# Optimization experiments

Measured on AMD Instinct MI355X. Metric: run time of the kernel, lower is better.

Reference implementation:

```python
import jax, jax.numpy as jnp
import numpy as np

N_NODES = 50000
N_EDGES = 800000
D_IN = 128
D_HID = 16
N_CLS = 3


def setup_inputs() -> dict:
    key = jax.random.key(0)
    k = jax.random.split(key, 8)
    x = jax.random.normal(k[0], (N_NODES, D_IN), dtype=jnp.float32)
    edge_index = jax.random.randint(k[1], (2, N_EDGES), 0, N_NODES, dtype=jnp.int64)
    # SAGEConv params: lin_l (applied to aggregated neighbors, has bias),
    # lin_r (applied to root node, no bias) -- PyG defaults with mean aggregation.
    s1 = 1.0 / np.sqrt(D_IN)
    s2 = 1.0 / np.sqrt(D_HID)
    W1_l = jax.random.normal(k[2], (D_HID, D_IN), dtype=jnp.float32) * s1
    b1_l = jnp.zeros((D_HID,), dtype=jnp.float32)
    W1_r = jax.random.normal(k[3], (D_HID, D_IN), dtype=jnp.float32) * s1
    W2_l = jax.random.normal(k[4], (N_CLS, D_HID), dtype=jnp.float32) * s2
    b2_l = jnp.zeros((N_CLS,), dtype=jnp.float32)
    W2_r = jax.random.normal(k[5], (N_CLS, D_HID), dtype=jnp.float32) * s2
    return {"x": x, "edge_index": edge_index, "W1_l": W1_l, "b1_l": b1_l,
            "W1_r": W1_r, "W2_l": W2_l, "b2_l": b2_l, "W2_r": W2_r}


def _mean_aggregate(x, src, dst, num_nodes):
    # messages x_j = x[src] scattered to dst, mean-reduced (PyG SAGEConv aggr='mean')
    summed = jax.ops.segment_sum(x[src], dst, num_segments=num_nodes)  # [N, D]
    counts = jax.ops.segment_sum(jnp.ones((src.shape[0],), dtype=x.dtype), dst,
                                 num_segments=num_nodes)
    return summed / jnp.maximum(counts, 1.0)[:, None]


def _sage_conv(x, src, dst, W_l, b_l, W_r, num_nodes):
    agg = _mean_aggregate(x, src, dst, num_nodes)
    return agg @ W_l.T + b_l + x @ W_r.T


def reference(x, edge_index, W1_l, b1_l, W1_r, W2_l, b2_l, W2_r):
    src, dst = edge_index[0], edge_index[1]
    n = x.shape[0]
    h = jax.nn.relu(_sage_conv(x, src, dst, W1_l, b1_l, W1_r, n))
    h = jax.nn.relu(_sage_conv(h, src, dst, W2_l, b2_l, W2_r, n))
    return jax.nn.log_softmax(h, axis=1)
```

## Files before the change

kernel.cpp:

```cpp
#include <hip/hip_runtime.h>
#include <math.h>

#define D_IN 128
#define N_CLS 3
#define NXCD 8
#define CAPU 64

__global__ __launch_bounds__(256) void zero_kernel(int* __restrict__ p, int n)
{
    int i = blockIdx.x * 256 + threadIdx.x;
    if (i < n) p[i] = 0;
}

__global__ __launch_bounds__(256) void pack_kernel(
    const int* __restrict__ src, const int* __restrict__ dstv,
    unsigned int* __restrict__ packed, int n_edges)
{
    int e = blockIdx.x * 256 + threadIdx.x;
    if (e < n_edges)
        packed[e] = ((unsigned)dstv[e] << 16) | (unsigned)src[e];
}

__global__ __launch_bounds__(256) void fused3_kernel(
    const float* __restrict__ x, const float* __restrict__ W1l,
    const float* __restrict__ W1r, float* __restrict__ y_l,
    float* __restrict__ y_r,
    const unsigned int* __restrict__ packed,
    int* __restrict__ deg, unsigned short* __restrict__ padadj,
    int n_edges, int n8, int n_nodes, int nblk)
{
    __shared__ float ws[32 * 132];
    const int t = threadIdx.x;

    for (int m = t; m < (32 * 128) / 4; m += 256) {
        int f = m * 4;
        int row = f >> 7, col = f & 127;
        const float* srcw = (row < 16) ? (W1l + row * 128 + col)
                                       : (W1r + (row - 16) * 128 + col);
        *(float4*)&ws[row * 132 + col] = *(const float4*)srcw;
    }
    __syncthreads();

    if (t < 128) {
        const int xg = blockIdx.x & (NXCD - 1);
        const int q  = blockIdx.x >> 3;
        const unsigned lo = (unsigned)(xg * n8);
        unsigned hi = lo + (unsigned)n8;
        if (hi > (unsigned)n_nodes) hi = (unsigned)n_nodes;
        const int gpb = nblk >> 3;
        const int stride = gpb * 128;
        const int e4n = n_edges >> 2;
        for (int i = q * 128 + t; i < e4n; i += stride) {
            uint4 p4 = *(const uint4*)&packed[i * 4];
            unsigned d, s;
            d = p4.x >> 16; s = p4.x & 0xFFFFu;
            if (d >= lo && d < hi) {
                int r = atomicAdd(&deg[d], 1);
                if (r < CAPU) padadj[(size_t)d * CAPU + r] = (unsigned short)s;
            }
            d = p4.y >> 16; s = p4.y & 0xFFFFu;
            if (d >= lo && d < hi) {
                int r = atomicAdd(&deg[d], 1);
                if (r < CAPU) padadj[(size_t)d * CAPU + r] = (unsigned short)s;
            }
            d = p4.z >> 16; s = p4.z & 0xFFFFu;
            if (d >= lo && d < hi) {
                int r = atomicAdd(&deg[d], 1);
                if (r < CAPU) padadj[(size_t)d * CAPU + r] = (unsigned short)s;
            }
            d = p4.w >> 16; s = p4.w & 0xFFFFu;
            if (d >= lo && d < hi) {
                int r = atomicAdd(&deg[d], 1);
                if (r < CAPU) padadj[(size_t)d * CAPU + r] = (unsigned short)s;
            }
        }
        if (q == 0 && t < (n_edges & 3)) {
            int e = (e4n << 2) + t;
            unsigned p = packed[e];
            unsigned d = p >> 16, s = p & 0xFFFFu;
            if (d >= lo && d < hi) {
                int r = atomicAdd(&deg[d], 1);
                if (r < CAPU) padadj[(size_t)d * CAPU + r] = (unsigned short)s;
            }
        }
        return;
    }

    const int tt = t - 128;
    const int ng = tt >> 3;
    const int og = tt & 7;
    const int node = blockIdx.x * 16 + ng;
    if (node >= n_nodes) return;

    const float4* xp = (const float4*)(x + (size_t)node * D_IN);
    float acc[4] = {0.f, 0.f, 0.f, 0.f};
    for (int k4 = 0; k4 < 32; ++k4) {
        float4 xv = xp[k4];
        const int kb = k4 * 4;
        #pragma unroll
        for (int j = 0; j < 4; ++j) {
            float4 wv = *(const float4*)&ws[(og + 8 * j) * 132 + kb];
            acc[j] = fmaf(xv.x, wv.x, acc[j]);
            acc[j] = fmaf(xv.y, wv.y, acc[j]);
            acc[j] = fmaf(xv.z, wv.z, acc[j]);
            acc[j] = fmaf(xv.w, wv.w, acc[j]);
        }
    }
    #pragma unroll
    for (int j = 0; j < 4; ++j) {
        int col = og + 8 * j;
        if (col < 16) y_l[(size_t)node * 16 + col] = acc[j];
        else          y_r[(size_t)node * 16 + (col - 16)] = acc[j];
    }
}

__global__ __launch_bounds__(256) void gather1u_kernel(
    const int* __restrict__ deg, const unsigned short* __restrict__ padadj,
    const float* __restrict__ y_l, const float* __restrict__ y_r,
    const float* __restrict__ b1, const float* __restrict__ W2l,
    const float* __restrict__ W2r, float* __restrict__ z_l,
    float* __restrict__ z_r, int n_nodes, int n8)
{
    const int t = threadIdx.x;
    const int c = t & 15;
    const int xg = blockIdx.x & (NXCD - 1);
    const int q = blockIdx.x >> 3;
    const int local = q * 16 + (t >> 4);
    if (local >= n8) return;
    const int n = xg * n8 + local;
    if (n >= n_nodes) return;

    const int dc = deg[n];
    const int dcl = dc < CAPU ? dc : CAPU;
    const unsigned short* ap = padadj + (size_t)n * CAPU;
    float acc = 0.f;
    int j = 0;
    for (; j + 8 <= dcl; j += 8) {
        uint4 v = *(const uint4*)(ap + j);
        int i0 = v.x & 0xFFFF, i1 = v.x >> 16;
        int i2 = v.y & 0xFFFF, i3 = v.y >> 16;
        int i4 = v.z & 0xFFFF, i5 = v.z >> 16;
        int i6 = v.w & 0xFFFF, i7 = v.w >> 16;
        float a0 = y_l[(size_t)i0 * 16 + c];
        float a1 = y_l[(size_t)i1 * 16 + c];
        float a2 = y_l[(size_t)i2 * 16 + c];
        float a3 = y_l[(size_t)i3 * 16 + c];
        float a4 = y_l[(size_t)i4 * 16 + c];
        float a5 = y_l[(size_t)i5 * 16 + c];
        float a6 = y_l[(size_t)i6 * 16 + c];
        float a7 = y_l[(size_t)i7 * 16 + c];
        acc += ((a0 + a1) + (a2 + a3)) + ((a4 + a5) + (a6 + a7));
    }
    for (; j < dcl; ++j) acc += y_l[(size_t)ap[j] * 16 + c];

    float inv = 1.0f / fmaxf((float)dc, 1.0f);
    float h = fmaxf(fmaf(acc, inv, b1[c] + y_r[(size_t)n * 16 + c]), 0.f);

    float zl[N_CLS], zr[N_CLS];
    #pragma unroll
    for (int o = 0; o < N_CLS; ++o) {
        float pl = h * W2l[o * 16 + c];
        float pr = h * W2r[o * 16 + c];
        #pragma unroll
        for (int d = 1; d < 16; d <<= 1) {
            pl += __shfl_xor(pl, d, 64);
            pr += __shfl_xor(pr, d, 64);
        }
        zl[o] = pl; zr[o] = pr;
    }
    if (c == 0) {
        *(float4*)&z_l[(size_t)n * 4] = make_float4(zl[0], zl[1], zl[2], 0.f);
        *(float4*)&z_r[(size_t)n * 4] = make_float4(zr[0], zr[1], zr[2], 0.f);
    }
}

__global__ __launch_bounds__(256) void gather2u_out_kernel(
    const int* __restrict__ deg, const unsigned short* __restrict__ padadj,
    const float* __restrict__ z_l, const float* __restrict__ z_r,
    const float* __restrict__ b2, float* __restrict__ out,
    int n_nodes, int n8)
{
    const int xg = blockIdx.x & (NXCD - 1);
    const int q = blockIdx.x >> 3;
    const int local = q * 256 + threadIdx.x;
    if (local >= n8) return;
    const int n = xg * n8 + local;
    if (n >= n_nodes) return;

    const int dc = deg[n];
    const int dcl = dc < CAPU ? dc : CAPU;
    const unsigned short* ap = padadj + (size_t)n * CAPU;
    float a0 = 0.f, a1 = 0.f, a2 = 0.f;
    int j = 0;
    for (; j + 8 <= dcl; j += 8) {
        uint4 v = *(const uint4*)(ap + j);
        int i0 = v.x & 0xFFFF, i1 = v.x >> 16;
        int i2 = v.y & 0xFFFF, i3 = v.y >> 16;
        int i4 = v.z & 0xFFFF, i5 = v.z >> 16;
        int i6 = v.w & 0xFFFF, i7 = v.w >> 16;
        float4 v0 = *(const float4*)&z_l[(size_t)i0 * 4];
        float4 v1 = *(const float4*)&z_l[(size_t)i1 * 4];
        float4 v2 = *(const float4*)&z_l[(size_t)i2 * 4];
        float4 v3 = *(const float4*)&z_l[(size_t)i3 * 4];
        float4 v4 = *(const float4*)&z_l[(size_t)i4 * 4];
        float4 v5 = *(const float4*)&z_l[(size_t)i5 * 4];
        float4 v6 = *(const float4*)&z_l[(size_t)i6 * 4];
        float4 v7 = *(const float4*)&z_l[(size_t)i7 * 4];
        a0 += ((v0.x + v1.x) + (v2.x + v3.x)) + ((v4.x + v5.x) + (v6.x + v7.x));
        a1 += ((v0.y + v1.y) + (v2.y + v3.y)) + ((v4.y + v5.y) + (v6.y + v7.y));
        a2 += ((v0.z + v1.z) + (v2.z + v3.z)) + ((v4.z + v5.z) + (v6.z + v7.z));
    }
    for (; j < dcl; ++j) {
        float4 v = *(const float4*)&z_l[(size_t)ap[j] * 4];
        a0 += v.x; a1 += v.y; a2 += v.z;
    }
    float inv = 1.0f / fmaxf((float)dc, 1.0f);
    float4 r = *(const float4*)&z_r[(size_t)n * 4];
    float v0 = fmaxf(fmaf(a0, inv, b2[0] + r.x), 0.f);
    float v1 = fmaxf(fmaf(a1, inv, b2[1] + r.y), 0.f);
    float v2 = fmaxf(fmaf(a2, inv, b2[2] + r.z), 0.f);
    float m = fmaxf(fmaxf(v0, v1), v2);
    float s = expf(v0 - m) + expf(v1 - m) + expf(v2 - m);
    float lse = m + logf(s);
    out[(size_t)n * 3 + 0] = v0 - lse;
    out[(size_t)n * 3 + 1] = v1 - lse;
    out[(size_t)n * 3 + 2] = v2 - lse;
}


__global__ __launch_bounds__(128) void lin1_kernel(
    const float* __restrict__ x, const float* __restrict__ W1l,
    const float* __restrict__ W1r, float* __restrict__ y_l,
    float* __restrict__ y_r, int* __restrict__ deg, int n_nodes)
{
    __shared__ float xs[64 * 132];
    __shared__ float ws[32 * 132];
    const int t = threadIdx.x;
    const int node0 = blockIdx.x * 64;

    {
        int i = blockIdx.x * 128 + t;
        if (i < n_nodes) deg[i] = 0;
    }

    for (int m = t; m < (32 * 128) / 4; m += 128) {
        int f = m * 4;
        int row = f >> 7, col = f & 127;
        const float* srcw = (row < 16) ? (W1l + row * 128 + col)
                                       : (W1r + (row - 16) * 128 + col);
        *(float4*)&ws[row * 132 + col] = *(const float4*)srcw;
    }
    for (int m = t; m < (64 * 128) / 4; m += 128) {
        int f = m * 4;
        int row = f >> 7, col = f & 127;
        int node = node0 + row;
        float4 g = make_float4(0.f, 0.f, 0.f, 0.f);
        if (node < n_nodes) g = *(const float4*)(x + (size_t)node * D_IN + col);
        *(float4*)&xs[row * 132 + col] = g;
    }
    __syncthreads();

    const int ng = t >> 3;
    const int og = t & 7;
    float acc[4][4];
    #pragma unroll
    for (int i = 0; i < 4; ++i)
        #pragma unroll
        for (int j = 0; j < 4; ++j) acc[i][j] = 0.f;

    for (int k = 0; k < 128; k += 4) {
        float4 xv[4], wv[4];
        #pragma unroll
        for (int i = 0; i < 4; ++i)
            xv[i] = *(const float4*)&xs[(ng + 16 * i) * 132 + k];
        #pragma unroll
        for (int j = 0; j < 4; ++j)
            wv[j] = *(const float4*)&ws[(og + 8 * j) * 132 + k];
        #pragma unroll
        for (int i = 0; i < 4; ++i)
            #pragma unroll
            for (int j = 0; j < 4; ++j) {
                acc[i][j] = fmaf(xv[i].x, wv[j].x, acc[i][j]);
                acc[i][j] = fmaf(xv[i].y, wv[j].y, acc[i][j]);
                acc[i][j] = fmaf(xv[i].z, wv[j].z, acc[i][j]);
                acc[i][j] = fmaf(xv[i].w, wv[j].w, acc[i][j]);
            }
    }

    #pragma unroll
    for (int i = 0; i < 4; ++i) {
        int node = node0 + ng + 16 * i;
        if (node >= n_nodes) continue;
        #pragma unroll
        for (int j = 0; j < 4; ++j) {
            int col = og + 8 * j;
            if (col < 16) y_l[(size_t)node * 16 + col] = acc[i][j];
            else          y_r[(size_t)node * 16 + (col - 16)] = acc[i][j];
        }
    }
}

__global__ __launch_bounds__(256) void fillx_kernel(
    const int* __restrict__ src, const int* __restrict__ dst,
    int* __restrict__ deg, int* __restrict__ padadj,
    int n_edges, int cap, int n8, int n_nodes, int bpx)
{
    const int xg = blockIdx.x & (NXCD - 1);
    const int q  = blockIdx.x >> 3;
    const int lo = xg * n8;
    int hi = lo + n8; if (hi > n_nodes) hi = n_nodes;
    const int stride = bpx * 256;

    const int e4n = n_edges >> 2;
    for (int i = q * 256 + threadIdx.x; i < e4n; i += stride) {
        int4 d4 = *(const int4*)&dst[i * 4];
        if (d4.x >= lo && d4.x < hi) {
            int r = atomicAdd(&deg[d4.x], 1);
            if (r < cap) padadj[(size_t)d4.x * cap + r] = src[i * 4 + 0];
        }
        if (d4.y >= lo && d4.y < hi) {
            int r = atomicAdd(&deg[d4.y], 1);
            if (r < cap) padadj[(size_t)d4.y * cap + r] = src[i * 4 + 1];
        }
        if (d4.z >= lo && d4.z < hi) {
            int r = atomicAdd(&deg[d4.z], 1);
            if (r < cap) padadj[(size_t)d4.z * cap + r] = src[i * 4 + 2];
        }
        if (d4.w >= lo && d4.w < hi) {
            int r = atomicAdd(&deg[d4.w], 1);
            if (r < cap) padadj[(size_t)d4.w * cap + r] = src[i * 4 + 3];
        }
    }
    if (q == 0 && threadIdx.x < (n_edges & 3)) {
        int e = (e4n << 2) + threadIdx.x;
        int d = dst[e];
        if (d >= lo && d < hi) {
            int r = atomicAdd(&deg[d], 1);
            if (r < cap) padadj[(size_t)d * cap + r] = src[e];
        }
    }
}

__global__ __launch_bounds__(256) void gather1x_kernel(
    const int* __restrict__ deg, const int* __restrict__ padadj,
    const float* __restrict__ y_l, const float* __restrict__ y_r,
    const float* __restrict__ b1, const float* __restrict__ W2l,
    const float* __restrict__ W2r, float* __restrict__ z_l,
    float* __restrict__ z_r, int n_nodes, int cap, int n8)
{
    const int t = threadIdx.x;
    const int c = t & 15;
    const int xg = blockIdx.x & (NXCD - 1);
    const int q = blockIdx.x >> 3;
    const int local = q * 16 + (t >> 4);
    if (local >= n8) return;
    const int n = xg * n8 + local;
    if (n >= n_nodes) return;

    const int dc = deg[n];
    const int* ap = padadj + (size_t)n * cap;
    float acc = 0.f;
    int j = 0;
    for (; j + 4 <= dc; j += 4) {
        int4 s4 = *(const int4*)(ap + j);
        float a0 = y_l[(size_t)s4.x * 16 + c];
        float a1 = y_l[(size_t)s4.y * 16 + c];
        float a2 = y_l[(size_t)s4.z * 16 + c];
        float a3 = y_l[(size_t)s4.w * 16 + c];
        acc += (a0 + a1) + (a2 + a3);
    }
    for (; j < dc; ++j) acc += y_l[(size_t)ap[j] * 16 + c];

    float inv = 1.0f / fmaxf((float)dc, 1.0f);
    float h = fmaxf(fmaf(acc, inv, b1[c] + y_r[(size_t)n * 16 + c]), 0.f);

    float zl[N_CLS], zr[N_CLS];
    #pragma unroll
    for (int o = 0; o < N_CLS; ++o) {
        float pl = h * W2l[o * 16 + c];
        float pr = h * W2r[o * 16 + c];
        #pragma unroll
        for (int d = 1; d < 16; d <<= 1) {
            pl += __shfl_xor(pl, d, 64);
            pr += __shfl_xor(pr, d, 64);
        }
        zl[o] = pl; zr[o] = pr;
    }
    if (c == 0) {
        *(float4*)&z_l[(size_t)n * 4] = make_float4(zl[0], zl[1], zl[2], 0.f);
        *(float4*)&z_r[(size_t)n * 4] = make_float4(zr[0], zr[1], zr[2], 0.f);
    }
}

__global__ __launch_bounds__(256) void gather2x_out_kernel(
    const int* __restrict__ deg, const int* __restrict__ padadj,
    const float* __restrict__ z_l, const float* __restrict__ z_r,
    const float* __restrict__ b2, float* __restrict__ out,
    int n_nodes, int cap, int n8)
{
    const int xg = blockIdx.x & (NXCD - 1);
    const int q = blockIdx.x >> 3;
    const int local = q * 256 + threadIdx.x;
    if (local >= n8) return;
    const int n = xg * n8 + local;
    if (n >= n_nodes) return;

    const int dc = deg[n];
    const int* ap = padadj + (size_t)n * cap;
    float a0 = 0.f, a1 = 0.f, a2 = 0.f;
    int j = 0;
    for (; j + 4 <= dc; j += 4) {
        int4 s4 = *(const int4*)(ap + j);
        float4 v0 = *(const float4*)&z_l[(size_t)s4.x * 4];
        float4 v1 = *(const float4*)&z_l[(size_t)s4.y * 4];
        float4 v2 = *(const float4*)&z_l[(size_t)s4.z * 4];
        float4 v3 = *(const float4*)&z_l[(size_t)s4.w * 4];
        a0 += (v0.x + v1.x) + (v2.x + v3.x);
        a1 += (v0.y + v1.y) + (v2.y + v3.y);
        a2 += (v0.z + v1.z) + (v2.z + v3.z);
    }
    for (; j < dc; ++j) {
        float4 v = *(const float4*)&z_l[(size_t)ap[j] * 4];
        a0 += v.x; a1 += v.y; a2 += v.z;
    }
    float inv = 1.0f / fmaxf((float)dc, 1.0f);
    float4 r = *(const float4*)&z_r[(size_t)n * 4];
    float v0 = fmaxf(fmaf(a0, inv, b2[0] + r.x), 0.f);
    float v1 = fmaxf(fmaf(a1, inv, b2[1] + r.y), 0.f);
    float v2 = fmaxf(fmaf(a2, inv, b2[2] + r.z), 0.f);
    float m = fmaxf(fmaxf(v0, v1), v2);
    float s = expf(v0 - m) + expf(v1 - m) + expf(v2 - m);
    float lse = m + logf(s);
    out[(size_t)n * 3 + 0] = v0 - lse;
    out[(size_t)n * 3 + 1] = v1 - lse;
    out[(size_t)n * 3 + 2] = v2 - lse;
}

extern "C" void kernel_launch(void* const* d_in, const int* in_sizes, int n_in,
                              void* d_out, int out_size, void* d_ws, size_t ws_size,
                              hipStream_t stream)
{
    const float* x   = (const float*)d_in[0];
    const int*   ei  = (const int*)d_in[1];
    const float* W1l = (const float*)d_in[2];
    const float* b1  = (const float*)d_in[3];
    const float* W1r = (const float*)d_in[4];
    const float* W2l = (const float*)d_in[5];
    const float* b2  = (const float*)d_in[6];
    const float* W2r = (const float*)d_in[7];

    const int N = in_sizes[0] / D_IN;
    const int E = in_sizes[1] / 2;
    const int* srcI = ei;
    const int* dstI = ei + E;

    float* fws  = (float*)d_ws;
    float* y_l  = fws;
    float* y_r  = y_l + (size_t)N * 16;
    float* z_l  = y_r + (size_t)N * 16;
    float* z_r  = z_l + (size_t)N * 4;
    int*   iws  = (int*)(z_r + (size_t)N * 4);

    const int n8 = (N + NXCD - 1) / NXCD;

    const size_t need_u = 160ULL * N + 4ULL * N + 2ULL * CAPU * N + 4ULL * E;

    if (N < 65536 && ws_size >= need_u) {
        int* deg = iws;
        unsigned short* padadj = (unsigned short*)(deg + N);
        unsigned int* packed = (unsigned int*)(padadj + (size_t)N * CAPU);

        int nblk = (N + 15) / 16;
        nblk = (nblk + 7) & ~7;

        zero_kernel<<<(N + 255) / 256, 256, 0, stream>>>(deg, N);
        pack_kernel<<<(E + 255) / 256, 256, 0, stream>>>(srcI, dstI, packed, E);
        fused3_kernel<<<nblk, 256, 0, stream>>>(x, W1l, W1r, y_l, y_r,
                                                packed, deg, padadj,
                                                E, n8, N, nblk);
        const int g1b = (n8 + 15) / 16;
        gather1u_kernel<<<NXCD * g1b, 256, 0, stream>>>(deg, padadj, y_l, y_r,
                                                        b1, W2l, W2r,
                                                        z_l, z_r, N, n8);
        const int g2b = (n8 + 255) / 256;
        gather2u_out_kernel<<<NXCD * g2b, 256, 0, stream>>>(deg, padadj,
                                                            z_l, z_r, b2,
                                                            (float*)d_out, N, n8);
    } else {
        const int bpx = 128;
        int CAPF = 64;
        if (ws_size < 160ULL * N + 4ULL * N + 256ULL * N) CAPF = 48;
        int* deg    = iws;
        int* padadj = deg + N;

        lin1_kernel<<<(N + 63) / 64, 128, 0, stream>>>(x, W1l, W1r, y_l, y_r,
                                                       deg, N);
        fillx_kernel<<<NXCD * bpx, 256, 0, stream>>>(srcI, dstI, deg, padadj,
                                                     E, CAPF, n8, N, bpx);
        const int g1b_ = (n8 + 15) / 16;
        gather1x_kernel<<<NXCD * g1b_, 256, 0, stream>>>(deg, padadj, y_l, y_r,
                                                         b1, W2l, W2r,
                                                         z_l, z_r, N, CAPF, n8);
        const int g2b_ = (n8 + 255) / 256;
        gather2x_out_kernel<<<NXCD * g2b_, 256, 0, stream>>>(deg, padadj,
                                                             z_l, z_r, b2,
                                                             (float*)d_out, N, CAPF, n8);
    }
}
```

Baseline: 81.77 us.

## Compact edges per XCD bucket with wave-scan, then fill adjacency separately

The zero and pack kernels are merged into one prep kernel that also zeroes the per-bucket cursors. The fused linear/partition kernel no longer does scattered per-node atomics. Instead each wavefront keeps its in-range edges with a warp prefix scan and one atomic per wave, appending them to 32 bucket buffers (8 XCD ranges x 4 sub-buckets). A new fillc kernel then reads each bucket and performs the per-node degree atomics and padded-adjacency writes with better locality. This trades fewer contended atomics inside the fused kernel for an extra kernel launch and an extra write and read of the compacted edge list.

Result: slower. 219.3 us (+168.2%).

```diff
diff --git a/kernel.cpp b/kernel.cpp
--- a/kernel.cpp
+++ b/kernel.cpp
@@ -4,30 +4,27 @@
 #define D_IN 128
 #define N_CLS 3
 #define NXCD 8
+#define NSUB 4
 #define CAPU 64
 
-__global__ __launch_bounds__(256) void zero_kernel(int* __restrict__ p, int n)
+__global__ __launch_bounds__(256) void prep_pack_kernel(
+    const int* __restrict__ src, const int* __restrict__ dstv,
+    unsigned int* __restrict__ packed, int* __restrict__ z,
+    int n_edges, int nz)
 {
     int i = blockIdx.x * 256 + threadIdx.x;
-    if (i < n) p[i] = 0;
-}
-
-__global__ __launch_bounds__(256) void pack_kernel(
-    const int* __restrict__ src, const int* __restrict__ dstv,
-    unsigned int* __restrict__ packed, int n_edges)
-{
-    int e = blockIdx.x * 256 + threadIdx.x;
-    if (e < n_edges)
-        packed[e] = ((unsigned)dstv[e] << 16) | (unsigned)src[e];
-}
-
-__global__ __launch_bounds__(256) void fused3_kernel(
+    if (i < n_edges)
+        packed[i] = ((unsigned)dstv[i] << 16) | (unsigned)src[i];
+    if (i < nz) z[i] = 0;
+}
+
+__global__ __launch_bounds__(256) void fusedc_kernel(
     const float* __restrict__ x, const float* __restrict__ W1l,
     const float* __restrict__ W1r, float* __restrict__ y_l,
     float* __restrict__ y_r,
     const unsigned int* __restrict__ packed,
-    int* __restrict__ deg, unsigned short* __restrict__ padadj,
-    int n_edges, int n8, int n_nodes, int nblk)
+    unsigned int* __restrict__ cbuf, int* __restrict__ cur32,
+    int csub, int n_edges, int n8, int n_nodes, int nblk)
 {
     __shared__ float ws[32 * 132];
     const int t = threadIdx.x;
@@ -42,45 +39,52 @@
     __syncthreads();
 
     if (t < 128) {
-        const int xg = blockIdx.x & (NXCD - 1);
-        const int q  = blockIdx.x >> 3;
+        const int xg  = blockIdx.x & (NXCD - 1);
+        const int q   = blockIdx.x >> 3;
+        const int sub = q & (NSUB - 1);
         const unsigned lo = (unsigned)(xg * n8);
         unsigned hi = lo + (unsigned)n8;
         if (hi > (unsigned)n_nodes) hi = (unsigned)n_nodes;
         const int gpb = nblk >> 3;
-        const int stride = gpb * 128;
+        const int tstride = gpb * 128;
+        const int gt = q * 128 + t;
+        const int lane = t & 63;
         const int e4n = n_edges >> 2;
-        for (int i = q * 128 + t; i < e4n; i += stride) {
+        unsigned int* mybuf = cbuf + (size_t)(xg * NSUB + sub) * csub;
+        int* cursor = &cur32[xg * NSUB + sub];
+
+        for (int i = gt; i < e4n; i += tstride) {
             uint4 p4 = *(const uint4*)&packed[i * 4];
-            unsigned d, s;
-            d = p4.x >> 16; s = p4.x & 0xFFFFu;
-            if (d >= lo && d < hi) {
-                int r = atomicAdd(&deg[d], 1);
-                if (r < CAPU) padadj[(size_t)d * CAPU + r] = (unsigned short)s;
+            unsigned dx = p4.x >> 16, dy = p4.y >> 16,
+                     dz = p4.z >> 16, dw = p4.w >> 16;
+            bool f0 = (dx >= lo && dx < hi);
+            bool f1 = (dy >= lo && dy < hi);
+            bool f2 = (dz >= lo && dz < hi);
+            bool f3 = (dw >= lo && dw < hi);
+            int cnt = (int)f0 + (int)f1 + (int)f2 + (int)f3;
+            int pre = cnt;
+            #pragma unroll
+            for (int dd = 1; dd < 64; dd <<= 1) {
+                int u = __shfl_up(pre, dd, 64);
+                if (lane >= dd) pre += u;
             }
-            d = p4.y >> 16; s = p4.y & 0xFFFFu;
-            if (d >= lo && d < hi) {
-                int r = atomicAdd(&deg[d], 1);
-                if (r < CAPU) padadj[(size_t)d * CAPU + r] = (unsigned short)s;
-            }
-            d = p4.z >> 16; s = p4.z & 0xFFFFu;
-            if (d >= lo && d < hi) {
-                int r = atomicAdd(&deg[d], 1);
-                if (r < CAPU) padadj[(size_t)d * CAPU + r] = (unsigned short)s;
-            }
-            d = p4.w >> 16; s = p4.w & 0xFFFFu;
-            if (d >= lo && d < hi) {
-                int r = atomicAdd(&deg[d], 1);
-                if (r < CAPU) padadj[(size_t)d * CAPU + r] = (unsigned short)s;
-            }
+            int total = __shfl(pre, 63, 64);
+            int base = 0;
+            if (lane == 63 && total > 0) base = atomicAdd(cursor, total);
+            base = __shfl(base, 63, 64);
+            int o = base + pre - cnt;
+            if (f0) mybuf[o++] = p4.x;
+            if (f1) mybuf[o++] = p4.y;
+            if (f2) mybuf[o++] = p4.z;
+            if (f3) mybuf[o++] = p4.w;
         }
         if (q == 0 && t < (n_edges & 3)) {
             int e = (e4n << 2) + t;
             unsigned p = packed[e];
-            unsigned d = p >> 16, s = p & 0xFFFFu;
+            unsigned d = p >> 16;
             if (d >= lo && d < hi) {
-                int r = atomicAdd(&deg[d], 1);
-                if (r < CAPU) padadj[(size_t)d * CAPU + r] = (unsigned short)s;
+                int pos = atomicAdd(cursor, 1);
+                mybuf[pos] = p;
             }
         }
         return;
@@ -111,6 +115,25 @@
         int col = og + 8 * j;
         if (col < 16) y_l[(size_t)node * 16 + col] = acc[j];
         else          y_r[(size_t)node * 16 + (col - 16)] = acc[j];
+    }
+}
+
+__global__ __launch_bounds__(256) void fillc_kernel(
+    const unsigned int* __restrict__ cbuf, const int* __restrict__ cur32,
+    int* __restrict__ deg, unsigned short* __restrict__ padadj, int csub)
+{
+    const int xg  = blockIdx.x & (NXCD - 1);
+    const int sub = (blockIdx.x >> 3) & (NSUB - 1);
+    const int q   = blockIdx.x >> 5;
+    const int ridx = xg * NSUB + sub;
+    const int cnt = cur32[ridx];
+    const unsigned int* my = cbuf + (size_t)ridx * csub;
+    const int stride = 32 * 256;
+    for (int i = q * 256 + threadIdx.x; i < cnt; i += stride) {
+        unsigned p = my[i];
+        unsigned d = p >> 16, s = p & 0xFFFFu;
+        int r = atomicAdd(&deg[d], 1);
+        if (r < CAPU) padadj[(size_t)d * CAPU + r] = (unsigned short)s;
     }
 }
 
@@ -463,21 +486,27 @@
 
     const int n8 = (N + NXCD - 1) / NXCD;
 
-    const size_t need_u = 160ULL * N + 4ULL * N + 2ULL * CAPU * N + 4ULL * E;
-
-    if (N < 65536 && ws_size >= need_u) {
+    const int csub = E / NSUB + 65536;
+    const size_t need_c = 160ULL * N + 4ULL * (N + 32) + 2ULL * CAPU * N +
+                          4ULL * E + 4ULL * NXCD * NSUB * (size_t)csub;
+
+    if (N < 65536 && ws_size >= need_c) {
         int* deg = iws;
-        unsigned short* padadj = (unsigned short*)(deg + N);
+        int* cur32 = deg + N;
+        unsigned short* padadj = (unsigned short*)(cur32 + 32);
         unsigned int* packed = (unsigned int*)(padadj + (size_t)N * CAPU);
+        unsigned int* cbuf = packed + E;
 
         int nblk = (N + 15) / 16;
         nblk = (nblk + 7) & ~7;
 
-        zero_kernel<<<(N + 255) / 256, 256, 0, stream>>>(deg, N);
-        pack_kernel<<<(E + 255) / 256, 256, 0, stream>>>(srcI, dstI, packed, E);
-        fused3_kernel<<<nblk, 256, 0, stream>>>(x, W1l, W1r, y_l, y_r,
-                                                packed, deg, padadj,
+        int prep_n = (E > N + 32 ? E : N + 32);
+        prep_pack_kernel<<<(prep_n + 255) / 256, 256, 0, stream>>>(
+            srcI, dstI, packed, deg, E, N + 32);
+        fusedc_kernel<<<nblk, 256, 0, stream>>>(x, W1l, W1r, y_l, y_r,
+                                                packed, cbuf, cur32, csub,
                                                 E, n8, N, nblk);
+        fillc_kernel<<<1024, 256, 0, stream>>>(cbuf, cur32, deg, padadj, csub);
         const int g1b = (n8 + 15) / 16;
         gather1u_kernel<<<NXCD * g1b, 256, 0, stream>>>(deg, padadj, y_l, y_r,
                                                         b1, W2l, W2r,
```
